# Optimization experiments

Hardware: AMD Instinct MI355X
Metric: run time of the kernel (lower is better)

## Reference

```python
import jax, jax.numpy as jnp
import numpy as np

B, S, D = 8, 1024, 1024
H, DK, DV = 16, 64, 64
OUT = 64  # out_size; W_o output dim = OUT * H = 1024


def setup_inputs() -> dict:
    key = jax.random.key(0)
    ks = jax.random.split(key, 8)
    queries = jax.random.normal(ks[0], (B, S, D), dtype=jnp.float32)
    keys = jax.random.normal(ks[1], (B, S, D), dtype=jnp.float32)
    values = jax.random.normal(ks[2], (B, S, D), dtype=jnp.float32)
    # Linear weights stored as [in, out] (no bias per bias=False)
    Wq = jax.random.normal(ks[3], (D, DK * H), dtype=jnp.float32) * 0.02
    Wk = jax.random.normal(ks[4], (D, DK * H), dtype=jnp.float32) * 0.02
    Wv = jax.random.normal(ks[5], (D, DV * H), dtype=jnp.float32) * 0.02
    Wo = jax.random.normal(ks[6], (DV * H, OUT * H), dtype=jnp.float32) * 0.02
    valid_lens = jax.random.randint(ks[7], (B,), 1, S + 1, dtype=jnp.int32)
    return {"queries": queries, "keys": keys, "values": values,
            "Wq": Wq, "Wk": Wk, "Wv": Wv, "Wo": Wo, "valid_lens": valid_lens}


def reference(queries, keys, values, Wq, Wk, Wv, Wo, valid_lens):
    b, s, _ = queries.shape
    # projections + transpose_qkv: [B,S,H*dh] -> [B,H,S,dh]
    q = (queries @ Wq).reshape(b, s, H, DK).transpose(0, 2, 1, 3)
    k = (keys @ Wk).reshape(b, keys.shape[1], H, DK).transpose(0, 2, 1, 3)
    v = (values @ Wv).reshape(b, values.shape[1], H, DV).transpose(0, 2, 1, 3)
    scale = DK ** 0.5  # epsilon = 0.0
    scores = jnp.einsum('bhqd,bhkd->bhqk', q, k) / scale
    # valid_lens masking on last axis: masked entries set to -1e6 (not -inf)
    kv_len = k.shape[2]
    mask = jnp.arange(kv_len)[None, None, None, :] < valid_lens[:, None, None, None]
    scores = jnp.where(mask, scores, -1e6)
    attn = jax.nn.softmax(scores, axis=-1)  # dropout p=0.0 -> identity
    out = jnp.einsum('bhqk,bhkd->bhqd', attn, v)
    # transpose_output: [B,H,S,dv] -> [B,S,H*dv]
    out = out.transpose(0, 2, 1, 3).reshape(b, s, H * DV)
    return out @ Wo
```

## Files before the change

kernel.cpp:

```cpp
#include <hip/hip_runtime.h>
#include <hip/hip_bf16.h>
#include <stdint.h>

typedef __bf16 bf16_t;
typedef __bf16 bf16x8 __attribute__((ext_vector_type(8)));
typedef float f32x4 __attribute__((ext_vector_type(4)));

#define B_  8
#define S_  1024
#define D_  1024
#define H_  16
#define DH_ 64

static __device__ __forceinline__ f32x4 mfma_bf16(bf16x8 a, bf16x8 b, f32x4 c) {
  return __builtin_amdgcn_mfma_f32_16x16x32_bf16(a, b, c, 0, 0, 0);
}

#define GLOAD_LDS16(g, l)                                                     \
  __builtin_amdgcn_global_load_lds(                                           \
      (const __attribute__((address_space(1))) void*)(g),                     \
      (__attribute__((address_space(3))) void*)(l), 16, 0, 0)

__global__ __launch_bounds__(256) void transpose4(
    const float* __restrict__ w0, const float* __restrict__ w1,
    const float* __restrict__ w2, const float* __restrict__ w3,
    bf16_t* __restrict__ t0, bf16_t* __restrict__ t1,
    bf16_t* __restrict__ t2, bf16_t* __restrict__ t3)
{
  __shared__ float tile[64][65];
  const float* src; bf16_t* dst;
  switch (blockIdx.z) {
    case 0: src = w0; dst = t0; break;
    case 1: src = w1; dst = t1; break;
    case 2: src = w2; dst = t2; break;
    default: src = w3; dst = t3; break;
  }
  const int tx = threadIdx.x & 63;
  const int ty = threadIdx.x >> 6;
  const int c0 = blockIdx.x * 64, r0 = blockIdx.y * 64;
#pragma unroll
  for (int r = ty; r < 64; r += 4)
    tile[r][tx] = src[(size_t)(r0 + r) * 1024 + c0 + tx];
  __syncthreads();
#pragma unroll
  for (int r = ty; r < 64; r += 4)
    dst[(size_t)(c0 + r) * 1024 + r0 + tx] = (bf16_t)tile[tx][r];
}

__global__ __launch_bounds__(256) void convert_qkv(
    const float* __restrict__ q, const float* __restrict__ k,
    const float* __restrict__ v,
    bf16_t* __restrict__ qo, bf16_t* __restrict__ ko, bf16_t* __restrict__ vo)
{
  const float* src; bf16_t* dst;
  switch (blockIdx.y) {
    case 0: src = q; dst = qo; break;
    case 1: src = k; dst = ko; break;
    default: src = v; dst = vo; break;
  }
  const size_t i = ((size_t)blockIdx.x * 256 + threadIdx.x) * 8;
  float4 a = *(const float4*)(src + i);
  float4 b = *(const float4*)(src + i + 4);
  bf16x8 o;
  o[0] = (bf16_t)a.x; o[1] = (bf16_t)a.y; o[2] = (bf16_t)a.z; o[3] = (bf16_t)a.w;
  o[4] = (bf16_t)b.x; o[5] = (bf16_t)b.y; o[6] = (bf16_t)b.z; o[7] = (bf16_t)b.w;
  *(bf16x8*)(dst + i) = o;
}

__global__ __launch_bounds__(256) void transposeV(
    const bf16_t* __restrict__ src, bf16_t* __restrict__ dst)
{
  __shared__ bf16_t t[64 * 72];
  const size_t base = (size_t)blockIdx.y * (64 * 1024);
  const int s0 = blockIdx.x * 64;
#pragma unroll
  for (int it = 0; it < 2; ++it) {
    const int c = it * 256 + threadIdx.x;
    const int r = c >> 3, col8 = (c & 7) * 8;
    bf16x8 v = *(const bf16x8*)(src + base + (size_t)(s0 + r) * 64 + col8);
    *(bf16x8*)(t + r * 72 + col8) = v;
  }
  __syncthreads();
#pragma unroll
  for (int it = 0; it < 2; ++it) {
    const int c = it * 256 + threadIdx.x;
    const int d = c >> 3, sc8 = (c & 7) * 8;
    bf16x8 v;
#pragma unroll
    for (int j = 0; j < 8; ++j) v[j] = t[(sc8 + j) * 72 + d];
    *(bf16x8*)(dst + base + (size_t)d * 1024 + s0 + sc8) = v;
  }
}

#define BM_G 256
#define BN_G 128
#define BK_G 32
#define KDIM 1024
#define NK_G (KDIM / BK_G)
#define AEL (BM_G * BK_G)
#define BEL (BN_G * BK_G)
#define LDS_BYTES ((2 * (AEL + BEL)) * 2)

template <int MODE>
__device__ __forceinline__ void gemm_core(
    const bf16_t* __restrict__ Ap,
    const bf16_t* __restrict__ Bp,
    void* __restrict__ Cp,
    bf16_t* smem, int tileM, int tileMloc, int tileN)
{
  bf16_t* const As = smem;
  bf16_t* const Bs = smem + 2 * AEL;

  const int tid  = threadIdx.x;
  const int wv   = tid >> 6;
  const int lane = tid & 63;
  const int wm   = wv >> 1;
  const int wn   = wv & 1;
  const int quad = lane >> 4;
  const int l15  = lane & 15;

  const int srow = tid >> 2;
  const int sg   = (((tid & 3) - (srow >> 1)) & 3) << 3;
  const bf16_t* gA = Ap + (size_t)(tileM * BM_G + srow) * KDIM + sg;
  const bf16_t* gB = Bp + (size_t)(tileN * BN_G + srow) * KDIM + sg;
  const int lw = wv * 512;

#define STAGE6(koff, buf) do {                                                 \
    GLOAD_LDS16(gA + (koff),                      As + (buf)*AEL + 0*2048 + lw); \
    GLOAD_LDS16(gA + (size_t)64  * KDIM + (koff), As + (buf)*AEL + 1*2048 + lw); \
    GLOAD_LDS16(gA + (size_t)128 * KDIM + (koff), As + (buf)*AEL + 2*2048 + lw); \
    GLOAD_LDS16(gA + (size_t)192 * KDIM + (koff), As + (buf)*AEL + 3*2048 + lw); \
    GLOAD_LDS16(gB + (koff),                      Bs + (buf)*BEL + 0*2048 + lw); \
    GLOAD_LDS16(gB + (size_t)64  * KDIM + (koff), Bs + (buf)*BEL + 1*2048 + lw); \
  } while (0)

  f32x4 acc[8][4];
#pragma unroll
  for (int mi = 0; mi < 8; ++mi)
#pragma unroll
    for (int ni = 0; ni < 4; ++ni)
      acc[mi][ni] = (f32x4){0.f, 0.f, 0.f, 0.f};

  STAGE6(0, 0);
  STAGE6(BK_G, 1);
  asm volatile("s_waitcnt vmcnt(6)" ::: "memory");
  __builtin_amdgcn_s_barrier();

  for (int t = 0; t < NK_G; ++t) {
    const int cbA = (t & 1) * AEL;
    const int cbB = (t & 1) * BEL;

    bf16x8 af[8], bfr[4];
#pragma unroll
    for (int ni = 0; ni < 4; ++ni) {
      const int row = wn * 64 + ni * 16 + l15;
      bfr[ni] = *(const bf16x8*)(Bs + cbB + row * BK_G + (((quad + (row >> 1)) & 3) << 3));
    }
#pragma unroll
    for (int mi = 0; mi < 8; ++mi) {
      const int row = wm * 128 + mi * 16 + l15;
      af[mi] = *(const bf16x8*)(As + cbA + row * BK_G + (((quad + (row >> 1)) & 3) << 3));
    }
    __builtin_amdgcn_s_setprio(1);
#pragma unroll
    for (int mi = 0; mi < 8; ++mi)
#pragma unroll
      for (int ni = 0; ni < 4; ++ni)
        acc[mi][ni] = mfma_bf16(af[mi], bfr[ni], acc[mi][ni]);
    __builtin_amdgcn_s_setprio(0);
    asm volatile("s_waitcnt lgkmcnt(0)" ::: "memory");
    __builtin_amdgcn_s_barrier();

    if (t + 2 < NK_G) {
      STAGE6((size_t)(t + 2) * BK_G, t & 1);
      asm volatile("s_waitcnt vmcnt(6)" ::: "memory");
    } else if (t + 2 == NK_G) {
      asm volatile("s_waitcnt vmcnt(0)" ::: "memory");
    }
    if (t + 1 < NK_G) {
      asm volatile("" ::: "memory");
      __builtin_amdgcn_s_barrier();
    }
  }
#undef STAGE6

#pragma unroll
  for (int mi = 0; mi < 8; ++mi) {
#pragma unroll
    for (int ni = 0; ni < 4; ++ni) {
#pragma unroll
      for (int r = 0; r < 4; ++r) {
        const int row = tileMloc * BM_G + wm * 128 + mi * 16 + quad * 4 + r;
        const int col = tileN * BN_G + wn * 64 + ni * 16 + l15;
        if (MODE == 0) {
          ((float*)Cp)[(size_t)row * 1024 + col] = acc[mi][ni][r];
        } else {
          const int b = row >> 10, s = row & 1023;
          const int h = col >> 6,  d = col & 63;
          ((bf16_t*)Cp)[(((size_t)(b * H_ + h) << 10) | s) * DH_ + d] =
              (bf16_t)acc[mi][ni][r];
        }
      }
    }
  }
}

__global__ __launch_bounds__(256, 2) void gemm_proj(
    const bf16_t* __restrict__ A, const bf16_t* __restrict__ Bw,
    bf16_t* __restrict__ Cb)
{
  extern __shared__ bf16_t smem[];
  const int xcd = blockIdx.x & 7;
  const int r   = blockIdx.x >> 3;
  const int tileN = r & 7;
  const int tileM = xcd * 12 + (r >> 3);
  const int seg = tileM >> 5;
  gemm_core<1>(A, Bw + ((size_t)seg << 20), (void*)(Cb + ((size_t)seg << 23)),
               smem, tileM, tileM & 31, tileN);
}

__global__ __launch_bounds__(256, 2) void gemm_out(
    const bf16_t* __restrict__ Ap, const bf16_t* __restrict__ Bp,
    float* __restrict__ Cp)
{
  extern __shared__ bf16_t smem[];
  const int xcd = blockIdx.x & 7;
  const int r   = blockIdx.x >> 3;
  const int tileN = r & 7;
  const int tileM = xcd * 4 + (r >> 3);
  gemm_core<0>(Ap, Bp, (void*)Cp, smem, tileM, tileM, tileN);
}

__global__ __launch_bounds__(256) void attn64(
    const bf16_t* __restrict__ Q,
    const bf16_t* __restrict__ Kv,
    const bf16_t* __restrict__ Vt,
    const int* __restrict__ valid_lens,
    bf16_t* __restrict__ O)
{
  const int h  = blockIdx.x;
  const int qt = blockIdx.y;
  const int b  = blockIdx.z;
  const int tid  = threadIdx.x;
  const int wave = tid >> 6;
  const int lane = tid & 63;
  const int quad = lane >> 4;
  const int l15  = lane & 15;

  const int L   = valid_lens[b];
  const int nkt = (L + 63) >> 6;

  const size_t base = ((size_t)(b * H_ + h)) * S_ * DH_;
  const bf16_t* Qp = Q  + base;
  const bf16_t* Kp = Kv + base;
  const bf16_t* Vp = Vt + base;

  __shared__ bf16_t KsA[64 * 32];
  __shared__ bf16_t KsB[64 * 32];
  __shared__ bf16_t VsA[64 * 32];
  __shared__ bf16_t VsB[64 * 32];
  __shared__ bf16_t Pb[4][16 * 72];
  bf16_t* const Pw = &Pb[wave][0];

  const int sr = tid >> 2;
  const int sj = (tid & 3) << 3;
  const int ldsOff = (wave * 64) * 8;

  const int qrow = qt * 64 + wave * 16 + l15;
  const bf16x8 qf0 = *(const bf16x8*)(Qp + (size_t)qrow * DH_ + quad * 8);
  const bf16x8 qf1 = *(const bf16x8*)(Qp + (size_t)qrow * DH_ + 32 + quad * 8);

  f32x4 o[4];
  float lsum[4];
#pragma unroll
  for (int r = 0; r < 4; ++r) {
    o[r] = (f32x4){0.f, 0.f, 0.f, 0.f};
    lsum[r] = 0.f;
  }

  for (int kt = 0; kt < nkt; ++kt) {
    const int k0 = kt * 64;

    __syncthreads();
    GLOAD_LDS16(Kp + (size_t)(k0 + sr) * DH_ + sj,      KsA + ldsOff);
    GLOAD_LDS16(Kp + (size_t)(k0 + sr) * DH_ + 32 + sj, KsB + ldsOff);
    GLOAD_LDS16(Vp + (size_t)sr * S_ + k0 + sj,         VsA + ldsOff);
    GLOAD_LDS16(Vp + (size_t)sr * S_ + k0 + 32 + sj,    VsB + ldsOff);
    __syncthreads();

    f32x4 sc[4];
#pragma unroll
    for (int n16 = 0; n16 < 4; ++n16) {
      const int row = (n16 * 16 + l15) * 32 + quad * 8;
      bf16x8 kf0 = *(const bf16x8*)(KsA + row);
      bf16x8 kf1 = *(const bf16x8*)(KsB + row);
      f32x4 s = (f32x4){0.f, 0.f, 0.f, 0.f};
      s = mfma_bf16(qf0, kf0, s);
      s = mfma_bf16(qf1, kf1, s);
      sc[n16] = s;
    }

    if (k0 + 64 <= L) {
#pragma unroll
      for (int n16 = 0; n16 < 4; ++n16) {
#pragma unroll
        for (int r = 0; r < 4; ++r) {
          const float p = __expf(sc[n16][r] * 0.125f);
          lsum[r] += p;
          Pw[(quad * 4 + r) * 72 + n16 * 16 + l15] = (bf16_t)p;
        }
      }
    } else {
#pragma unroll
      for (int n16 = 0; n16 < 4; ++n16) {
        const bool valid = (k0 + n16 * 16 + l15) < L;
#pragma unroll
        for (int r = 0; r < 4; ++r) {
          const float p = valid ? __expf(sc[n16][r] * 0.125f) : 0.f;
          lsum[r] += p;
          Pw[(quad * 4 + r) * 72 + n16 * 16 + l15] = (bf16_t)p;
        }
      }
    }

    const bf16x8 pf0 = *(const bf16x8*)(Pw + l15 * 72 + quad * 8);
    const bf16x8 pf1 = *(const bf16x8*)(Pw + l15 * 72 + 32 + quad * 8);
#pragma unroll
    for (int dt = 0; dt < 4; ++dt) {
      const int row = (dt * 16 + l15) * 32 + quad * 8;
      bf16x8 vf0 = *(const bf16x8*)(VsA + row);
      bf16x8 vf1 = *(const bf16x8*)(VsB + row);
      o[dt] = mfma_bf16(pf0, vf0, o[dt]);
      o[dt] = mfma_bf16(pf1, vf1, o[dt]);
    }
  }

  float inv[4];
#pragma unroll
  for (int r = 0; r < 4; ++r) {
    float t = lsum[r];
    t += __shfl_xor(t, 1, 64);
    t += __shfl_xor(t, 2, 64);
    t += __shfl_xor(t, 4, 64);
    t += __shfl_xor(t, 8, 64);
    inv[r] = 1.f / t;
  }
  const int qout = qt * 64 + wave * 16 + quad * 4;
#pragma unroll
  for (int dt = 0; dt < 4; ++dt) {
#pragma unroll
    for (int r = 0; r < 4; ++r) {
      const float v = o[dt][r] * inv[r];
      O[((size_t)(b * S_ + qout + r)) * (H_ * DH_) + h * DH_ + dt * 16 + l15] = (bf16_t)v;
    }
  }
}

extern "C" void kernel_launch(void* const* d_in, const int* in_sizes, int n_in,
                              void* d_out, int out_size, void* d_ws, size_t ws_size,
                              hipStream_t stream) {
  const float* queries = (const float*)d_in[0];
  const float* keys    = (const float*)d_in[1];
  const float* values  = (const float*)d_in[2];
  const float* Wq      = (const float*)d_in[3];
  const float* Wk      = (const float*)d_in[4];
  const float* Wv      = (const float*)d_in[5];
  const float* Wo      = (const float*)d_in[6];
  const int* valid_lens = (const int*)d_in[7];
  float* out = (float*)d_out;

  bf16_t* ws = (bf16_t*)d_ws;
  const size_t MB = 1024 * 1024;
  bf16_t* WqT = ws + 0 * MB;
  bf16_t* WkT = ws + 1 * MB;
  bf16_t* WvT = ws + 2 * MB;
  bf16_t* WoT = ws + 3 * MB;
  bf16_t* Qc  = ws + 4 * MB;
  bf16_t* Kc  = ws + 12 * MB;
  bf16_t* Vc  = ws + 20 * MB;
  bf16_t* Qb  = ws + 28 * MB;
  bf16_t* Kb  = ws + 36 * MB;
  bf16_t* Vb  = ws + 44 * MB;
  bf16_t* VbT = ws + 52 * MB;
  bf16_t* Ab  = ws + 60 * MB;

  (void)hipFuncSetAttribute((const void*)gemm_proj,
                            hipFuncAttributeMaxDynamicSharedMemorySize, LDS_BYTES);
  (void)hipFuncSetAttribute((const void*)gemm_out,
                            hipFuncAttributeMaxDynamicSharedMemorySize, LDS_BYTES);

  transpose4<<<dim3(16, 16, 4), 256, 0, stream>>>(Wq, Wk, Wv, Wo, WqT, WkT, WvT, WoT);

  convert_qkv<<<dim3(4096, 3), 256, 0, stream>>>(queries, keys, values, Qc, Kc, Vc);

  gemm_proj<<<dim3(768, 1, 1), 256, LDS_BYTES, stream>>>(Qc, WqT, Qb);

  transposeV<<<dim3(16, 128), 256, 0, stream>>>(Vb, VbT);

  attn64<<<dim3(16, 16, 8), 256, 0, stream>>>(Qb, Kb, VbT, valid_lens, Ab);

  gemm_out<<<dim3(256, 1, 1), 256, LDS_BYTES, stream>>>(Ab, WoT, out);
}
```

Measured before the change: 291.9 us.

## Merge prep kernels and write V projection transposed directly from GEMM epilogue

Measured after the change: 315.8 us. 8.2% more time.

```diff
diff --git a/kernel.cpp b/kernel.cpp
--- a/kernel.cpp
+++ b/kernel.cpp
@@ -21,74 +21,54 @@
       (const __attribute__((address_space(1))) void*)(g),                     \
       (__attribute__((address_space(3))) void*)(l), 16, 0, 0)
 
-__global__ __launch_bounds__(256) void transpose4(
+__global__ __launch_bounds__(256) void prep(
+    const float* __restrict__ q, const float* __restrict__ k,
+    const float* __restrict__ v,
     const float* __restrict__ w0, const float* __restrict__ w1,
     const float* __restrict__ w2, const float* __restrict__ w3,
+    bf16_t* __restrict__ qo, bf16_t* __restrict__ ko, bf16_t* __restrict__ vo,
     bf16_t* __restrict__ t0, bf16_t* __restrict__ t1,
     bf16_t* __restrict__ t2, bf16_t* __restrict__ t3)
 {
   __shared__ float tile[64][65];
-  const float* src; bf16_t* dst;
-  switch (blockIdx.z) {
-    case 0: src = w0; dst = t0; break;
-    case 1: src = w1; dst = t1; break;
-    case 2: src = w2; dst = t2; break;
-    default: src = w3; dst = t3; break;
-  }
-  const int tx = threadIdx.x & 63;
-  const int ty = threadIdx.x >> 6;
-  const int c0 = blockIdx.x * 64, r0 = blockIdx.y * 64;
-#pragma unroll
-  for (int r = ty; r < 64; r += 4)
-    tile[r][tx] = src[(size_t)(r0 + r) * 1024 + c0 + tx];
-  __syncthreads();
-#pragma unroll
-  for (int r = ty; r < 64; r += 4)
-    dst[(size_t)(c0 + r) * 1024 + r0 + tx] = (bf16_t)tile[tx][r];
-}
-
-__global__ __launch_bounds__(256) void convert_qkv(
-    const float* __restrict__ q, const float* __restrict__ k,
-    const float* __restrict__ v,
-    bf16_t* __restrict__ qo, bf16_t* __restrict__ ko, bf16_t* __restrict__ vo)
-{
-  const float* src; bf16_t* dst;
-  switch (blockIdx.y) {
-    case 0: src = q; dst = qo; break;
-    case 1: src = k; dst = ko; break;
-    default: src = v; dst = vo; break;
-  }
-  const size_t i = ((size_t)blockIdx.x * 256 + threadIdx.x) * 8;
-  float4 a = *(const float4*)(src + i);
-  float4 b = *(const float4*)(src + i + 4);
-  bf16x8 o;
-  o[0] = (bf16_t)a.x; o[1] = (bf16_t)a.y; o[2] = (bf16_t)a.z; o[3] = (bf16_t)a.w;
-  o[4] = (bf16_t)b.x; o[5] = (bf16_t)b.y; o[6] = (bf16_t)b.z; o[7] = (bf16_t)b.w;
-  *(bf16x8*)(dst + i) = o;
-}
-
-__global__ __launch_bounds__(256) void transposeV(
-    const bf16_t* __restrict__ src, bf16_t* __restrict__ dst)
-{
-  __shared__ bf16_t t[64 * 72];
-  const size_t base = (size_t)blockIdx.y * (64 * 1024);
-  const int s0 = blockIdx.x * 64;
-#pragma unroll
-  for (int it = 0; it < 2; ++it) {
-    const int c = it * 256 + threadIdx.x;
-    const int r = c >> 3, col8 = (c & 7) * 8;
-    bf16x8 v = *(const bf16x8*)(src + base + (size_t)(s0 + r) * 64 + col8);
-    *(bf16x8*)(t + r * 72 + col8) = v;
-  }
-  __syncthreads();
-#pragma unroll
-  for (int it = 0; it < 2; ++it) {
-    const int c = it * 256 + threadIdx.x;
-    const int d = c >> 3, sc8 = (c & 7) * 8;
-    bf16x8 v;
-#pragma unroll
-    for (int j = 0; j < 8; ++j) v[j] = t[(sc8 + j) * 72 + d];
-    *(bf16x8*)(dst + base + (size_t)d * 1024 + s0 + sc8) = v;
+  const int bx = blockIdx.x;
+  if (bx < 1024) {
+    const int z = bx >> 8, rem = bx & 255;
+    const int gx = rem & 15, gy = rem >> 4;
+    const float* src; bf16_t* dst;
+    switch (z) {
+      case 0: src = w0; dst = t0; break;
+      case 1: src = w1; dst = t1; break;
+      case 2: src = w2; dst = t2; break;
+      default: src = w3; dst = t3; break;
+    }
+    const int tx = threadIdx.x & 63;
+    const int ty = threadIdx.x >> 6;
+    const int c0 = gx * 64, r0 = gy * 64;
+#pragma unroll
+    for (int r = ty; r < 64; r += 4)
+      tile[r][tx] = src[(size_t)(r0 + r) * 1024 + c0 + tx];
+    __syncthreads();
+#pragma unroll
+    for (int r = ty; r < 64; r += 4)
+      dst[(size_t)(c0 + r) * 1024 + r0 + tx] = (bf16_t)tile[tx][r];
+  } else {
+    const int idx = bx - 1024;
+    const int zy = idx >> 12;
+    const int gx = idx & 4095;
+    const float* src; bf16_t* dst;
+    switch (zy) {
+      case 0: src = q; dst = qo; break;
+      case 1: src = k; dst = ko; break;
+      default: src = v; dst = vo; break;
+    }
+    const size_t i = ((size_t)gx * 256 + threadIdx.x) * 8;
+    float4 a = *(const float4*)(src + i);
+    float4 b = *(const float4*)(src + i + 4);
+    bf16x8 o;
+    o[0] = (bf16_t)a.x; o[1] = (bf16_t)a.y; o[2] = (bf16_t)a.z; o[3] = (bf16_t)a.w;
+    o[4] = (bf16_t)b.x; o[5] = (bf16_t)b.y; o[6] = (bf16_t)b.z; o[7] = (bf16_t)b.w;
+    *(bf16x8*)(dst + i) = o;
   }
 }
 
@@ -106,7 +86,7 @@
     const bf16_t* __restrict__ Ap,
     const bf16_t* __restrict__ Bp,
     void* __restrict__ Cp,
-    bf16_t* smem, int tileM, int tileMloc, int tileN)
+    bf16_t* smem, int tileM, int tileMloc, int tileN, int vt)
 {
   bf16_t* const As = smem;
   bf16_t* const Bs = smem + 2 * AEL;
@@ -197,8 +177,13 @@
         } else {
           const int b = row >> 10, s = row & 1023;
           const int h = col >> 6,  d = col & 63;
-          ((bf16_t*)Cp)[(((size_t)(b * H_ + h) << 10) | s) * DH_ + d] =
-              (bf16_t)acc[mi][ni][r];
+          if (vt) {
+            ((bf16_t*)Cp)[(((size_t)((b * H_ + h) * 64 + d)) << 10) | s] =
+                (bf16_t)acc[mi][ni][r];
+          } else {
+            ((bf16_t*)Cp)[(((size_t)(b * H_ + h) << 10) | s) * DH_ + d] =
+                (bf16_t)acc[mi][ni][r];
+          }
         }
       }
     }
@@ -207,7 +192,7 @@
 
 __global__ __launch_bounds__(256, 2) void gemm_proj(
     const bf16_t* __restrict__ A, const bf16_t* __restrict__ Bw,
-    bf16_t* __restrict__ Cb)
+    bf16_t* __restrict__ Cqk, bf16_t* __restrict__ Vt)
 {
   extern __shared__ bf16_t smem[];
   const int xcd = blockIdx.x & 7;
@@ -215,8 +200,10 @@
   const int tileN = r & 7;
   const int tileM = xcd * 12 + (r >> 3);
   const int seg = tileM >> 5;
-  gemm_core<1>(A, Bw + ((size_t)seg << 20), (void*)(Cb + ((size_t)seg << 23)),
-               smem, tileM, tileM & 31, tileN);
+  const int vt  = (seg == 2);
+  bf16_t* Cp = vt ? Vt : (Cqk + ((size_t)seg << 23));
+  gemm_core<1>(A, Bw + ((size_t)seg << 20), (void*)Cp,
+               smem, tileM, tileM & 31, tileN, vt);
 }
 
 __global__ __launch_bounds__(256, 2) void gemm_out(
@@ -228,7 +215,7 @@
   const int r   = blockIdx.x >> 3;
   const int tileN = r & 7;
   const int tileM = xcd * 4 + (r >> 3);
-  gemm_core<0>(Ap, Bp, (void*)Cp, smem, tileM, tileM, tileN);
+  gemm_core<0>(Ap, Bp, (void*)Cp, smem, tileM, tileM, tileN, 0);
 }
 
 __global__ __launch_bounds__(256) void attn64(
@@ -379,8 +366,6 @@
   bf16_t* Kc  = ws + 12 * MB;
   bf16_t* Vc  = ws + 20 * MB;
   bf16_t* Qb  = ws + 28 * MB;
-  bf16_t* Kb  = ws + 36 * MB;
-  bf16_t* Vb  = ws + 44 * MB;
   bf16_t* VbT = ws + 52 * MB;
   bf16_t* Ab  = ws + 60 * MB;
 
@@ -389,15 +374,13 @@
   (void)hipFuncSetAttribute((const void*)gemm_out,
                             hipFuncAttributeMaxDynamicSharedMemorySize, LDS_BYTES);
 
-  transpose4<<<dim3(16, 16, 4), 256, 0, stream>>>(Wq, Wk, Wv, Wo, WqT, WkT, WvT, WoT);
-
-  convert_qkv<<<dim3(4096, 3), 256, 0, stream>>>(queries, keys, values, Qc, Kc, Vc);
-
-  gemm_proj<<<dim3(768, 1, 1), 256, LDS_BYTES, stream>>>(Qc, WqT, Qb);
-
-  transposeV<<<dim3(16, 128), 256, 0, stream>>>(Vb, VbT);
-
-  attn64<<<dim3(16, 16, 8), 256, 0, stream>>>(Qb, Kb, VbT, valid_lens, Ab);
+  prep<<<dim3(1024 + 12288, 1, 1), 256, 0, stream>>>(
+      queries, keys, values, Wq, Wk, Wv, Wo,
+      Qc, Kc, Vc, WqT, WkT, WvT, WoT);
+
+  gemm_proj<<<dim3(768, 1, 1), 256, LDS_BYTES, stream>>>(Qc, WqT, Qb, VbT);
+
+  attn64<<<dim3(16, 16, 8), 256, 0, stream>>>(Qb, Qb + 8 * MB, VbT, valid_lens, Ab);
 
   gemm_out<<<dim3(256, 1, 1), 256, LDS_BYTES, stream>>>(Ab, WoT, out);
 }
```
